# Kernel optimization log

Measured on AMD Instinct MI355X. Metric: run time of the kernel, lower is better.

## Reference

```python
import jax, jax.numpy as jnp
import numpy as np

B, N, M, DC, NUM_ITERS = 64, 1024, 512, 6, 5
# leave-one-out index table: row j lists the DC-1 positions != j
LOO = np.array([[k for k in range(DC) if k != j] for j in range(DC)])  # [DC, DC-1]


def setup_inputs() -> dict:
    key = jax.random.key(0)
    k1, k2, k3, k4 = jax.random.split(key, 4)
    rng = np.random.default_rng(0)
    # row-regular sparse parity-check matrix: each check touches exactly DC variables
    row_cols = np.stack([np.sort(rng.choice(N, DC, replace=False)) for _ in range(M)]).astype(np.int32)
    H = np.zeros((M, N), np.float32)
    H[np.arange(M)[:, None], row_cols] = 1.0
    soft_input = jax.random.normal(k1, (B, N), jnp.float32) * 2.0  # channel LLRs
    labels = jax.random.randint(k2, (B, N), 0, 2).astype(jnp.int64)
    # neural_network_process: Dense(4) then Dense(1), no bias, non-negative weights
    W1 = jnp.abs(jax.random.normal(k3, (DC - 1, 4), jnp.float32)) * 0.3
    W2 = jnp.abs(jax.random.normal(k4, (4, 1), jnp.float32)) * 0.3
    bit_w1 = jnp.full((1,), -0.048, jnp.float32)
    bit_w2 = jnp.full((1,), -0.048, jnp.float32)
    return dict(soft_input=soft_input, labels=labels, H=jnp.asarray(H),
                row_cols=jnp.asarray(row_cols), W1=W1, W2=W2,
                bit_w1=bit_w1, bit_w2=bit_w2)


def reference(soft_input, labels, H, row_cols, W1, W2, bit_w1, bit_w2):
    # NMS-r belief propagation: NUM_ITERS iterations of vc update, check-node
    # update via sorted leave-one-out magnitudes fed to a tiny non-neg NN,
    # and marginalization. Returns all soft outputs [NUM_ITERS+1, B, N].
    rows = jnp.arange(M)[:, None]                 # [M,1] for gather/scatter
    sp1 = jax.nn.softplus(bit_w1)                 # bit weight 1 (compute_vc)
    sp2 = jax.nn.softplus(bit_w2)                 # bit weight 2 (marginalize)
    loo = jnp.asarray(LOO)

    def body(cv, _):
        # compute_vc
        temp = cv.sum(axis=1) + soft_input * sp1  # [B,N]
        vc = temp[:, None, :] * H - cv            # [B,M,N]
        # compute_cv1: sign part
        s = jnp.sign((1.0 - H)[None] + vc)        # +1 at H==0 positions
        result_sign = jnp.prod(s, axis=-1)[..., None] * H * s
        # magnitude part: gather the DC nonzeros per check row
        nz = jnp.abs(vc)[:, rows, row_cols]       # [B,M,DC]
        srt = jnp.sort(nz[..., loo], axis=-1)     # [B,M,DC,DC-1] sorted ascending
        vals = ((srt @ W1) @ W2)[..., 0]          # tiny NN -> [B,M,DC]
        cv_dense = jnp.zeros_like(vc).at[:, rows, row_cols].set(vals)
        cv_new = jax.lax.stop_gradient(result_sign) * cv_dense
        # marginalize
        soft_out = cv_new.sum(axis=1) + sp2 * soft_input
        return cv_new, soft_out

    cv0 = jnp.zeros((soft_input.shape[0], M, N), jnp.float32)
    _, outs = jax.lax.scan(body, cv0, None, length=NUM_ITERS)
    return jnp.concatenate([soft_input[None], outs], axis=0)  # soft_output_list
```

## Files before the change

kernel.cpp:

```cpp
#include <hip/hip_runtime.h>


constexpr int BB    = 64;
constexpr int NCOL  = 1024;
constexpr int MROW  = 512;
constexpr int KDC   = 6;
constexpr int ITERS = 5;
constexpr int THR   = 512;

__device__ __forceinline__ float softplusf(float x) {
    return fmaxf(x, 0.f) + log1pf(expf(-fabsf(x)));
}
__device__ __forceinline__ float sgnf(float x) {
    return (x > 0.f) ? 1.f : ((x < 0.f) ? -1.f : 0.f);
}

__global__ void __launch_bounds__(THR) k_decode(
        const float* __restrict__ soft,
        const int*   __restrict__ row_cols,
        const float* __restrict__ W1,
        const float* __restrict__ W2,
        const float* __restrict__ bw1,
        const float* __restrict__ bw2,
        float* __restrict__ out) {
    __shared__ float T[NCOL];
    __shared__ float S[NCOL];

    const int b   = blockIdx.x;
    const int tid = threadIdx.x;
    const int m   = tid;
    const int n0  = tid;
    const int n1  = tid + THR;

    const float sp1 = softplusf(bw1[0]);
    const float sp2 = softplusf(bw2[0]);

    float w[KDC - 1];
#pragma unroll
    for (int j = 0; j < KDC - 1; ++j) {
        float a = 0.f;
#pragma unroll
        for (int q = 0; q < 4; ++q) a += W1[j * 4 + q] * W2[q];
        w[j] = a;
    }

    const float* sb = soft + b * NCOL;
    const float s0 = sb[n0], s1 = sb[n1];
    out[b * NCOL + n0] = s0;
    out[b * NCOL + n1] = s1;
    T[n0] = sp1 * s0;  T[n1] = sp1 * s1;
    S[n0] = 0.f;       S[n1] = 0.f;

    int   cols[KDC];
    float cv[KDC];
#pragma unroll
    for (int k = 0; k < KDC; ++k) {
        cols[k] = row_cols[m * KDC + k];
        cv[k]   = 0.f;
    }
    __syncthreads();

#pragma unroll
    for (int p = 0; p < ITERS; ++p) {
        float sg[KDC], mag[KDC], P = 1.f;
#pragma unroll
        for (int k = 0; k < KDC; ++k) {
            float v = T[cols[k]] - cv[k];
            float s = sgnf(v);
            sg[k] = s;  P *= s;
            mag[k] = fabsf(v);
        }
        int rank[KDC];
#pragma unroll
        for (int k = 0; k < KDC; ++k) {
            int r = 0;
#pragma unroll
            for (int j = 0; j < KDC; ++j)
                r += (mag[j] < mag[k]) || (mag[j] == mag[k] && j < k);
            rank[k] = r;
        }
        float srt[KDC];
#pragma unroll
        for (int r = 0; r < KDC; ++r) {
            float v = 0.f;
#pragma unroll
            for (int k = 0; k < KDC; ++k) v = (rank[k] == r) ? mag[k] : v;
            srt[r] = v;
        }
        float pre[KDC];
        pre[0] = 0.f;
#pragma unroll
        for (int r = 0; r < KDC - 1; ++r) pre[r + 1] = pre[r] + srt[r] * w[r];
        float suf[KDC];
        suf[KDC - 1] = 0.f;
#pragma unroll
        for (int r = KDC - 2; r >= 0; --r) suf[r] = suf[r + 1] + srt[r + 1] * w[r];
        float valr[KDC];
#pragma unroll
        for (int r = 0; r < KDC; ++r) valr[r] = pre[r] + suf[r];

#pragma unroll
        for (int k = 0; k < KDC; ++k) {
            float val = 0.f;
#pragma unroll
            for (int r = 0; r < KDC; ++r) val = (rank[k] == r) ? valr[r] : val;
            float cvn = P * sg[k] * val;
            cv[k] = cvn;
            atomicAdd(&S[cols[k]], cvn);
        }
        __syncthreads();

        float a0 = S[n0], a1 = S[n1];
        float* op = out + (size_t)(p + 1) * (BB * NCOL) + b * NCOL;
        op[n0] = fmaf(sp2, s0, a0);
        op[n1] = fmaf(sp2, s1, a1);
        T[n0] = fmaf(sp1, s0, a0);
        T[n1] = fmaf(sp1, s1, a1);
        S[n0] = 0.f;  S[n1] = 0.f;
        __syncthreads();
    }
}

extern "C" void kernel_launch(void* const* d_in, const int* in_sizes, int n_in,
                              void* d_out, int out_size, void* d_ws, size_t ws_size,
                              hipStream_t stream) {
    const float* soft     = (const float*)d_in[0];
    const int*   row_cols = (const int*)d_in[3];
    const float* W1       = (const float*)d_in[4];
    const float* W2       = (const float*)d_in[5];
    const float* bw1      = (const float*)d_in[6];
    const float* bw2      = (const float*)d_in[7];
    float* out = (float*)d_out;

    k_decode<<<dim3(BB), dim3(THR), 0, stream>>>(soft, row_cols, W1, W2,
                                                 bw1, bw2, out);
}
```

Baseline: 91.92 us.

## Triple-buffer check sums to drop a barrier and sort edges with a network

Rotates three shared accumulator buffers per iteration, so reading the previous sums, zeroing the next buffer and accumulating the current one can share a single barrier per iteration instead of two. Variable-to-check values are computed on the fly from the previous sum plus the scaled channel LLR. The rank-and-select sort is replaced by a compare-exchange sorting network that permutes values and column indices together, which removes the scatter back to original positions. This uses more shared memory, and the column order in registers changes between iterations, which is fine because cv is permuted along with it.

```diff
diff --git a/kernel.cpp b/kernel.cpp
--- a/kernel.cpp
+++ b/kernel.cpp
@@ -3,10 +3,10 @@
 
 constexpr int BB    = 64;
 constexpr int NCOL  = 1024;
-constexpr int MROW  = 512;
 constexpr int KDC   = 6;
 constexpr int ITERS = 5;
 constexpr int THR   = 512;
+constexpr int TOT   = BB * NCOL;
 
 __device__ __forceinline__ float softplusf(float x) {
     return fmaxf(x, 0.f) + log1pf(expf(-fabsf(x)));
@@ -23,14 +23,12 @@
         const float* __restrict__ bw1,
         const float* __restrict__ bw2,
         float* __restrict__ out) {
-    __shared__ float T[NCOL];
-    __shared__ float S[NCOL];
+    __shared__ float SPS[NCOL];
+    __shared__ float S[3][NCOL];
 
+    const int tid = threadIdx.x;
     const int b   = blockIdx.x;
-    const int tid = threadIdx.x;
-    const int m   = tid;
-    const int n0  = tid;
-    const int n1  = tid + THR;
+    const int n0  = tid, n1 = tid + THR;
 
     const float sp1 = softplusf(bw1[0]);
     const float sp2 = softplusf(bw2[0]);
@@ -48,77 +46,74 @@
     const float s0 = sb[n0], s1 = sb[n1];
     out[b * NCOL + n0] = s0;
     out[b * NCOL + n1] = s1;
-    T[n0] = sp1 * s0;  T[n1] = sp1 * s1;
-    S[n0] = 0.f;       S[n1] = 0.f;
+    SPS[n0] = sp1 * s0;  SPS[n1] = sp1 * s1;
+    S[1][n0] = 0.f;      S[1][n1] = 0.f;
 
     int   cols[KDC];
     float cv[KDC];
 #pragma unroll
     for (int k = 0; k < KDC; ++k) {
-        cols[k] = row_cols[m * KDC + k];
+        cols[k] = row_cols[tid * KDC + k];
         cv[k]   = 0.f;
     }
     __syncthreads();
 
 #pragma unroll
     for (int p = 0; p < ITERS; ++p) {
-        float sg[KDC], mag[KDC], P = 1.f;
+        const int rd = p % 3, ac = (p + 1) % 3, zr = (p + 2) % 3;
+
+        float v[KDC];
 #pragma unroll
         for (int k = 0; k < KDC; ++k) {
-            float v = T[cols[k]] - cv[k];
-            float s = sgnf(v);
-            sg[k] = s;  P *= s;
-            mag[k] = fabsf(v);
+            const int c = cols[k];
+            v[k] = (p == 0) ? SPS[c] : (S[rd][c] + SPS[c] - cv[k]);
         }
-        int rank[KDC];
+
+        if (p >= 1) {
+            const float a0 = S[rd][n0], a1 = S[rd][n1];
+            float* op = out + (size_t)p * TOT + b * NCOL;
+            op[n0] = fmaf(sp2, s0, a0);
+            op[n1] = fmaf(sp2, s1, a1);
+        }
+        S[zr][n0] = 0.f;  S[zr][n1] = 0.f;
+
+#define CE(i, j) { bool sw = fabsf(v[i]) > fabsf(v[j]);                  \
+        float tv = sw ? v[j] : v[i]; v[j] = sw ? v[i] : v[j]; v[i] = tv; \
+        int tc = sw ? cols[j] : cols[i];                                  \
+        cols[j] = sw ? cols[i] : cols[j]; cols[i] = tc; }
+        CE(0,1)
+        CE(1,2) CE(0,1)
+        CE(2,3) CE(1,2) CE(0,1)
+        CE(3,4) CE(2,3) CE(1,2) CE(0,1)
+        CE(4,5) CE(3,4) CE(2,3) CE(1,2) CE(0,1)
+#undef CE
+
+        float mr[KDC], sg[KDC];
 #pragma unroll
-        for (int k = 0; k < KDC; ++k) {
-            int r = 0;
-#pragma unroll
-            for (int j = 0; j < KDC; ++j)
-                r += (mag[j] < mag[k]) || (mag[j] == mag[k] && j < k);
-            rank[k] = r;
-        }
-        float srt[KDC];
-#pragma unroll
-        for (int r = 0; r < KDC; ++r) {
-            float v = 0.f;
-#pragma unroll
-            for (int k = 0; k < KDC; ++k) v = (rank[k] == r) ? mag[k] : v;
-            srt[r] = v;
-        }
+        for (int r = 0; r < KDC; ++r) { sg[r] = sgnf(v[r]); mr[r] = fabsf(v[r]); }
+        const float P = sg[0] * sg[1] * sg[2] * sg[3] * sg[4] * sg[5];
+
         float pre[KDC];
         pre[0] = 0.f;
 #pragma unroll
-        for (int r = 0; r < KDC - 1; ++r) pre[r + 1] = pre[r] + srt[r] * w[r];
+        for (int r = 0; r < KDC - 1; ++r) pre[r + 1] = pre[r] + mr[r] * w[r];
         float suf[KDC];
         suf[KDC - 1] = 0.f;
 #pragma unroll
-        for (int r = KDC - 2; r >= 0; --r) suf[r] = suf[r + 1] + srt[r + 1] * w[r];
-        float valr[KDC];
-#pragma unroll
-        for (int r = 0; r < KDC; ++r) valr[r] = pre[r] + suf[r];
+        for (int r = KDC - 2; r >= 0; --r) suf[r] = suf[r + 1] + mr[r + 1] * w[r];
 
 #pragma unroll
-        for (int k = 0; k < KDC; ++k) {
-            float val = 0.f;
-#pragma unroll
-            for (int r = 0; r < KDC; ++r) val = (rank[k] == r) ? valr[r] : val;
-            float cvn = P * sg[k] * val;
-            cv[k] = cvn;
-            atomicAdd(&S[cols[k]], cvn);
+        for (int r = 0; r < KDC; ++r) {
+            const float cvn = P * sg[r] * (pre[r] + suf[r]);
+            cv[r] = cvn;
+            atomicAdd(&S[ac][cols[r]], cvn);
         }
         __syncthreads();
+    }
 
-        float a0 = S[n0], a1 = S[n1];
-        float* op = out + (size_t)(p + 1) * (BB * NCOL) + b * NCOL;
-        op[n0] = fmaf(sp2, s0, a0);
-        op[n1] = fmaf(sp2, s1, a1);
-        T[n0] = fmaf(sp1, s0, a0);
-        T[n1] = fmaf(sp1, s1, a1);
-        S[n0] = 0.f;  S[n1] = 0.f;
-        __syncthreads();
-    }
+    float* op = out + (size_t)ITERS * TOT + b * NCOL;
+    op[n0] = fmaf(sp2, s0, S[ITERS % 3][n0]);
+    op[n1] = fmaf(sp2, s1, S[ITERS % 3][n1]);
 }
 
 extern "C" void kernel_launch(void* const* d_in, const int* in_sizes, int n_in,
```

Measured after the change: 90.44 us. About the same (-1.6%).
